# Kernel optimization log

Measured on AMD Instinct MI355X. Metric: run time of the kernel, lower is better.

The kernel has to match this reference:

```python
import jax, jax.numpy as jnp
import numpy as np

NU, NI, G, D, HD, OD = 8000, 10000, 4096, 64, 64, 64
ALPHA = 0.8      # self vs neighbor mixing in NodeApplyModule
EPS = 1e-8       # cosine-similarity denominator epsilon
NEG_BIG = -1e38  # replacement for all -inf rows


def setup_inputs() -> dict:
    key = jax.random.key(0)
    ks = jax.random.split(key, 24)
    def lin(k, o, i):
        return (jax.random.normal(k, (o, i), jnp.float32) * 0.02)
    def bias(k, o):
        return (jax.random.normal(k, (o,), jnp.float32) * 0.02)
    inp = {}
    inp["H"] = jax.random.randint(ks[0], (NU + NI, G), 0, 2, jnp.int32)
    inp["feats_weight"] = jax.random.normal(ks[1], (NU + NI, D), jnp.float32) * 0.1
    inp["num_groups"] = G
    # user SelfAttention params
    inp["u_Wq"] = lin(ks[2], HD, D); inp["u_bq"] = bias(ks[3], HD)
    inp["u_Wk"] = lin(ks[4], HD, D); inp["u_bk"] = bias(ks[5], HD)
    inp["u_Wv"] = lin(ks[6], HD, D); inp["u_bv"] = bias(ks[7], HD)
    inp["u_Ws"] = lin(ks[8], 1, NU); inp["u_bs"] = bias(ks[9], 1)
    # item SelfAttention params
    inp["i_Wq"] = lin(ks[10], HD, D); inp["i_bq"] = bias(ks[11], HD)
    inp["i_Wk"] = lin(ks[12], HD, D); inp["i_bk"] = bias(ks[13], HD)
    inp["i_Wv"] = lin(ks[14], HD, D); inp["i_bv"] = bias(ks[15], HD)
    inp["i_Ws"] = lin(ks[16], 1, NI); inp["i_bs"] = bias(ks[17], 1)
    # WeightedGCN NodeApplyModule linear: in_feats = 2*HD -> out_feats = OD
    inp["g_W"] = lin(ks[18], OD, 2 * HD); inp["g_b"] = bias(ks[19], OD)
    return inp


def _self_attention(x, mask, num_groups, Wq, bq, Wk, bk, Wv, bv, Ws, bs):
    # x: [N, D] ; mask: [N, G]
    q = x @ Wq.T + bq            # [N, HD]
    k = x @ Wk.T + bk            # [N, HD]
    v = x @ Wv.T + bv            # [N, HD]
    s = (q @ k.T) @ Ws.T + bs    # [N, 1]  (Linear(num_elem,1) over q@k.T)
    scores = jnp.broadcast_to(s.reshape(1, -1), (num_groups, x.shape[0]))  # [G, N]
    maskT = (mask == 0).T        # [G, N]
    scores = jnp.where(maskT, -jnp.inf, scores)
    all_inf = jnp.all(scores == -jnp.inf, axis=1, keepdims=True)
    scores = jnp.where(all_inf, jnp.float32(NEG_BIG), scores)
    w = jax.nn.softmax(scores, axis=1)   # [G, N]
    return w @ v, w                      # [G, HD], [G, N]


def reference(H, feats_weight, num_groups,
              u_Wq, u_bq, u_Wk, u_bk, u_Wv, u_bv, u_Ws, u_bs,
              i_Wq, i_bq, i_Wk, i_bk, i_Wv, i_bv, i_Ws, i_bs,
              g_W, g_b):
    users_feats = feats_weight[:NU]
    items_feats = feats_weight[NU:]
    users_mask = H[:NU]
    items_mask = H[NU:]

    gf_u, w_u = _self_attention(users_feats, users_mask, num_groups,
                                u_Wq, u_bq, u_Wk, u_bk, u_Wv, u_bv, u_Ws, u_bs)
    gf_i, w_i = _self_attention(items_feats, items_mask, num_groups,
                                i_Wq, i_bq, i_Wk, i_bk, i_Wv, i_bv, i_Ws, i_bs)
    # NaN scrubbing (faithful to torch.where(isnan, 0, .))
    gf_i = jnp.where(jnp.isnan(gf_i), 0.0, gf_i)
    w_i = jnp.where(jnp.isnan(w_i), 0.0, w_i)

    group_weights = jnp.concatenate([w_u, w_i], axis=1)   # [G, NU+NI]
    group_feats = jnp.concatenate([gf_u, gf_i], axis=1)   # [G, 2*HD]

    # similarity graph (cosine similarity of group weight rows)
    wp = group_weights @ group_weights.T                  # [G, G]
    norms = jnp.sqrt(jnp.sum(group_weights * group_weights, axis=1))
    l2 = 1.0 / (norms[:, None] * norms[None, :] + EPS)
    A = wp * l2  # edge weight src->dst at A[src, dst]; zero WP entries contribute 0

    # weighted mean aggregation (DGL msg/reduce: sum(w*h)/sum(w) over in-edges)
    msg = A.T @ group_feats                 # [G, 2*HD]: sum_src A[src,dst]*h[src]
    deg = jnp.sum(A, axis=0)[:, None]       # [G, 1]:   sum_src A[src,dst]
    h_neigh = jnp.where(deg > 0, msg / jnp.where(deg > 0, deg, 1.0), 0.0)

    agg = ALPHA * group_feats + (1.0 - ALPHA) * h_neigh
    out = jax.nn.sigmoid(agg @ g_W.T + g_b)               # [G, OD]
    return out
```

## Files before the change

### kernel.cpp

```cpp
#include <hip/hip_runtime.h>
#include <hip/hip_bf16.h>
#include <cstdint>
#include <cstddef>

#define NU   8000
#define NI   10000
#define NTOT 18000
#define G    4096
#define KP2  18176
#define NSL  284
#define NSL128 142
#define KT8  142
#define UT8  63
#define KP2B 2272
#define GB8  512

typedef __attribute__((ext_vector_type(4))) float f32x4;

__device__ __forceinline__ float bfu(unsigned short u){
  return __uint_as_float(((unsigned)u)<<16);
}
__device__ __forceinline__ unsigned short f2b(float f){
  __hip_bfloat16 h = __float2bfloat16(f);
  return __builtin_bit_cast(unsigned short, h);
}
__device__ __forceinline__ unsigned char f2f8(float v){
  int p = __builtin_amdgcn_cvt_pk_fp8_f32(v, 0.f, 0, false);
  return (unsigned char)(p & 0xff);
}
template<int SEL>
__device__ __forceinline__ float f8tof(unsigned int w){
  return __builtin_amdgcn_cvt_f32_fp8((int)w, SEL);
}
__device__ __forceinline__ void async16(void* lds, const void* g){
  __builtin_amdgcn_global_load_lds((const __attribute__((address_space(1))) unsigned int*)g,
                                   (__attribute__((address_space(3))) unsigned int*)lds, 16, 0, 0);
}
__device__ __forceinline__ int slot2n(int s){
  return (s < 8064) ? (s < 8000 ? s : -1) : (s-64 < NTOT ? s-64 : -1);
}
__device__ __forceinline__ unsigned int mask4(unsigned int n){
  return ((n*0x00204081u)&0x01010101u)*0xFFu;
}

__global__ __launch_bounds__(256) void k_proj(
    const float* __restrict__ feats,
    const float* uWq, const float* ubq, const float* uWk, const float* ubk,
    const float* uWv, const float* ubv, const float* uWs,
    const float* iWq, const float* ibq, const float* iWk, const float* ibk,
    const float* iWv, const float* ibv, const float* iWs,
    float* __restrict__ q, unsigned short* __restrict__ vrow, float* __restrict__ wsk)
{
  __shared__ unsigned short Wt[6*4096];
  __shared__ float bl[6*64];
  __shared__ float wacc[128];
  const float* mats[6]  = {uWq,uWk,uWv,iWq,iWk,iWv};
  const float* bias6[6] = {ubq,ubk,ubv,ibq,ibk,ibv};
  int t = threadIdx.x;
  for (int m=0;m<6;m++)
    for (int e=t; e<4096; e+=256){
      int dd = e>>6, jj = e&63;
      Wt[m*4096 + jj*64 + dd] = f2b(mats[m][e]);
    }
  for (int e=t; e<384; e+=256) bl[e] = bias6[e>>6][e&63];
  if (t<128) wacc[t]=0.f;
  __syncthreads();
  int wave=t>>6, lane=t&63;
  int gw = blockIdx.x*4+wave, nw = gridDim.x*4;
  float accU=0.f, accI=0.f;
  for (int n=gw; n<NTOT; n+=nw){
    int br = (n>=NU);
    const unsigned short* W = Wt + br*3*4096;
    const float* bb = bl + br*192;
    float x = feats[(size_t)n*64+lane];
    float qd=bb[lane], kd=bb[64+lane], vd=bb[128+lane];
    #pragma unroll 16
    for (int j=0;j<64;j++){
      float xj = __shfl(x, j, 64);
      qd += xj * bfu(W[       j*64+lane]);
      kd += xj * bfu(W[4096 + j*64+lane]);
      vd += xj * bfu(W[8192 + j*64+lane]);
    }
    q[(size_t)n*64+lane] = qd;
    vrow[(size_t)n*64+lane] = f2b(vd);
    float wsn = br ? iWs[n-NU] : uWs[n];
    if (br) accI += wsn*kd; else accU += wsn*kd;
  }
  atomicAdd(&wacc[lane], accU);
  atomicAdd(&wacc[64+lane], accI);
  __syncthreads();
  if (t<128) atomicAdd(&wsk[t], wacc[t]);
}

__global__ __launch_bounds__(256) void k_score(const float* __restrict__ q, const float* __restrict__ wsk,
    const float* ubs, const float* ibs, float* __restrict__ rfs, unsigned char* __restrict__ rbs)
{
  __shared__ float wl[128];
  __shared__ float bs2[2];
  int t=threadIdx.x;
  if (t<128) wl[t]=wsk[t];
  if (t==128) bs2[0]=ubs[0];
  if (t==129) bs2[1]=ibs[0];
  __syncthreads();
  int wave=t>>6, lane=t&63;
  #pragma unroll 4
  for (int i=0;i<32;i++){
    int slot = blockIdx.x*128 + i*4 + wave;
    int n = slot2n(slot);
    int br = (slot>=8064);
    float v = 0.f;
    if (n>=0) v = q[(size_t)n*64+lane] * wl[br*64+lane];
    #pragma unroll
    for (int m=32;m>=1;m>>=1) v += __shfl_xor(v, m, 64);
    if (lane==0){
      if (n>=0){
        unsigned char b = f2f8(expf(v + bs2[br]));
        rbs[slot]=b; rfs[slot]=f8tof<0>((unsigned int)b);
      } else {
        rbs[slot]=0; rfs[slot]=0.f;
      }
    }
  }
}

__global__ __launch_bounds__(256) void k_buildB(
    const int* __restrict__ H, const float* __restrict__ rfs,
    unsigned char* __restrict__ Wb, unsigned char* __restrict__ Wbt,
    float* __restrict__ Zu, float* __restrict__ Zi,
    float* __restrict__ S2u, float* __restrict__ S2i)
{
  __shared__ __align__(16) unsigned char Bt[128][16];
  __shared__ float rl[128];
  __shared__ float zp[16][128];
  __shared__ float sp[16][128];
  int t = threadIdx.x;
  int s0 = blockIdx.x*128, g0 = blockIdx.y*128;
  int isItem = (s0 >= 8064);
  if (t<128){ int n = slot2n(s0+t); rl[t] = (n>=0)? rfs[s0+t] : 0.f; }
  __syncthreads();
  int gb = t&15, rbase = t>>4;
  float za[8]={0.f,0.f,0.f,0.f,0.f,0.f,0.f,0.f};
  float sa[8]={0.f,0.f,0.f,0.f,0.f,0.f,0.f,0.f};
  #pragma unroll
  for (int i=0;i<8;i++){
    int row = rbase + i*16;
    int n = slot2n(s0+row);
    unsigned int b8 = 0;
    if (n>=0){
      const int* hp = H + (size_t)n*G + g0 + gb*8;
      int4 h0 = *(const int4*)hp;
      int4 h1 = *(const int4*)(hp+4);
      float rq = rl[row], rq2 = rq*rq;
      if (h0.x){ b8|=1u;    za[0]+=rq; sa[0]+=rq2; }
      if (h0.y){ b8|=2u;    za[1]+=rq; sa[1]+=rq2; }
      if (h0.z){ b8|=4u;    za[2]+=rq; sa[2]+=rq2; }
      if (h0.w){ b8|=8u;    za[3]+=rq; sa[3]+=rq2; }
      if (h1.x){ b8|=16u;   za[4]+=rq; sa[4]+=rq2; }
      if (h1.y){ b8|=32u;   za[5]+=rq; sa[5]+=rq2; }
      if (h1.z){ b8|=64u;   za[6]+=rq; sa[6]+=rq2; }
      if (h1.w){ b8|=128u;  za[7]+=rq; sa[7]+=rq2; }
    }
    Bt[row][gb] = (unsigned char)b8;
  }
  #pragma unroll
  for (int j=0;j<8;j++){ zp[rbase][gb*8+j]=za[j]; sp[rbase][gb*8+j]=sa[j]; }
  __syncthreads();
  {
    int row = t>>1, half = t&1;
    *(unsigned long long*)(Wbt + (size_t)(s0+row)*GB8 + (g0>>3) + half*8) =
        *(const unsigned long long*)(&Bt[row][half*8]);
  }
  {
    int g = t>>1, sh = t&1;
    int gB = g>>3, gs = g&7;
    unsigned long long ob = 0;
    #pragma unroll
    for (int sb=0; sb<8; sb++){
      int base = (sh*8+sb)*8;
      unsigned int x = 0;
      #pragma unroll
      for (int j=0;j<8;j++) x |= (((unsigned int)(Bt[base+j][gB]) >> gs)&1u) << j;
      ob |= (unsigned long long)x << (sb*8);
    }
    *(unsigned long long*)(Wb + (size_t)(g0+g)*KP2B + (s0>>3) + sh*8) = ob;
  }
  if (t<128){
    float z=0.f, s2=0.f;
    #pragma unroll
    for (int j=0;j<16;j++){ z += zp[j][t]; s2 += sp[j][t]; }
    if (isItem){ atomicAdd(&Zi[g0+t], z); atomicAdd(&S2i[g0+t], s2); }
    else       { atomicAdd(&Zu[g0+t], z); atomicAdd(&S2u[g0+t], s2); }
  }
}

__global__ __launch_bounds__(256) void k_mid(
    const float* __restrict__ Zu, const float* __restrict__ Zi,
    const float* __restrict__ S2u, const float* __restrict__ S2i,
    float* __restrict__ Cu, float* __restrict__ Ci,
    float* __restrict__ cnu, float* __restrict__ cni, float* __restrict__ ninv,
    unsigned char* __restrict__ cn8u, unsigned char* __restrict__ cn8i,
    unsigned char* __restrict__ Wb, unsigned char* __restrict__ Wbt,
    const unsigned short* __restrict__ vrow, unsigned char* __restrict__ vt8)
{
  __shared__ unsigned short tile[64][65];
  int b = blockIdx.x;
  int t = threadIdx.x;
  if (b == 0){
    for (int g=t; g<G; g+=256){
      float zu=Zu[g], zi=Zi[g];
      int fu = !(zu>0.f), fi = !(zi>0.f);
      float cu = fu ? (1.f/(float)NU) : 1.f/zu;
      float ci = fi ? (1.f/(float)NI) : 1.f/zi;
      float nu  = fu ? (1.f/(float)NU) : S2u[g]*cu*cu;
      float ni_ = fi ? (1.f/(float)NI) : S2i[g]*ci*ci;
      float nv = rsqrtf(nu+ni_);
      Cu[g]=cu; Ci[g]=ci; ninv[g]=nv; cnu[g]=cu*nv; cni[g]=ci*nv;
      cn8u[g] = f2f8(cu*nv*64.f);
      cn8i[g] = f2f8(ci*nv*64.f);
      if (fu){
        for (int k=0;k<1000;k++) Wb[(size_t)g*KP2B+k]=0xFF;
        for (int k=0;k<NU;k++)
          atomicOr((unsigned*)Wbt + (((size_t)k*GB8 + (g>>3))>>2), 1u<<((g&7) + 8*((g>>3)&3)));
      }
      if (fi){
        for (int k=1008;k<2258;k++) Wb[(size_t)g*KP2B+k]=0xFF;
        for (int k=8064;k<18064;k++)
          atomicOr((unsigned*)Wbt + (((size_t)k*GB8 + (g>>3))>>2), 1u<<((g&7) + 8*((g>>3)&3)));
      }
    }
    return;
  }
  int s0 = (b-1)*64;
  int tc = t&63, tr = t>>6;
  #pragma unroll
  for (int i=0;i<16;i++){
    int row = tr+i*4;
    int n = slot2n(s0+row);
    tile[row][tc] = (n>=0) ? vrow[(size_t)n*64+tc] : (unsigned short)0;
  }
  __syncthreads();
  int dOff = (s0 >= 8064) ? 64 : 0;
  #pragma unroll
  for (int i=0;i<16;i++){
    int dd = tr+i*4;
    float v = bfu(tile[tc][dd]) * 16.f;
    vt8[(size_t)(dOff+dd)*KP2 + s0+tc] = f2f8(v);
  }
}

template<int MODE>
__global__ __launch_bounds__(256) void k_gemm(
    const unsigned char* __restrict__ A, const unsigned char* __restrict__ B,
    float* __restrict__ Cs, float* __restrict__ degsl,
    const unsigned char* __restrict__ u8,
    const unsigned char* __restrict__ cn8u, const unsigned char* __restrict__ cn8i,
    float* __restrict__ uslice, const unsigned char* __restrict__ rbsg,
    long ldF, long ldc)
{
  __shared__ __align__(16) unsigned char BufF[2][16384];
  __shared__ __align__(16) unsigned char BufB[2][2048];
  __shared__ __align__(16) unsigned char AuxR[2][1024];
  __shared__ unsigned int RowDw[128];
  int t=threadIdx.x, wave=t>>6, lane=t&63;
  int I=blockIdx.x, J=blockIdx.y, z=blockIdx.z;
  int kt0=0, ktn=0;
  if (MODE==0){ kt0 = z*9; ktn = min(9, KT8-kt0); }
  else if (MODE==1){ kt0 = z*8; ktn = 8; }
  else {
    if (z<8){ kt0 = z*8;             ktn = min(8, UT8-kt0); }
    else    { kt0 = UT8 + (z-8)*10;  ktn = min(10, KT8-kt0); }
  }
  f32x4 acc[4][4];
  #pragma unroll
  for (int mi=0;mi<4;mi++)
    #pragma unroll
    for (int ni=0;ni<4;ni++){
      acc[mi][ni][0]=0.f; acc[mi][ni][1]=0.f; acc[mi][ni][2]=0.f; acc[mi][ni][3]=0.f;
    }
  f32x4 accd[4];
  if (MODE==2){
    #pragma unroll
    for (int mi=0;mi<4;mi++){ accd[mi][0]=0.f; accd[mi][1]=0.f; accd[mi][2]=0.f; accd[mi][3]=0.f; }
  }
  f32x4 accu[4];
  if (MODE==1){
    #pragma unroll
    for (int ni=0;ni<4;ni++){ accu[ni][0]=0.f; accu[ni][1]=0.f; accu[ni][2]=0.f; accu[ni][3]=0.f; }
  }
  int l7 = lane&7, q4 = lane>>4, cl15 = lane&15;
  int rowOff = wave*8 + (lane>>3);
  int cchunk = (lane&7) ^ ((lane>>3)&7);
  long aRow0 = (MODE==1) ? ((J>=UT8)?128:0) : 0;
  const unsigned char* Fbase;
  const unsigned char* Bitbase;
  if (MODE==1){ Fbase = A + aRow0*ldF + (long)cchunk*16; Bitbase = B + (long)J*128*GB8; }
  else        { Fbase = B + (long)cchunk*16;             Bitbase = A + (long)I*128*KP2B; }
  const unsigned char* cnrow = (MODE==1) ? ((J>=UT8) ? cn8i : cn8u) : nullptr;
  int mrow0 = (wave&1)*64, nrow0 = (wave>>1)*64;

  if (MODE==1 && t<128) RowDw[t] = 0x01010101u * (unsigned int)rbsg[(size_t)J*128 + t];

  auto STAGE = [&](int buf, int kt){
    long k0 = (long)kt*128;
    #pragma unroll
    for (int rr=0; rr<4; rr++)
      async16(BufF[buf] + wave*1024 + rr*4096, Fbase + (long)(rr*32 + rowOff)*ldF + k0);
    if (wave<2)
      async16(BufB[buf] + wave*1024, Bitbase + (long)(wave*64+lane)*(MODE==1?GB8:KP2B) + (long)kt*16);
    if (MODE!=1 && wave==2)
      async16(AuxR[buf], rbsg + (long)kt*128 + (long)(lane&7)*16);
  };

  STAGE(0, kt0);
  __syncthreads();

  for (int kt=kt0; kt<kt0+ktn; ++kt){
    int cur = (kt - kt0) & 1;
    if (kt+1 < kt0+ktn) STAGE(cur^1, kt+1);
    const unsigned char* Fb = BufF[cur];
    const unsigned char* Bb = BufB[cur];
    #pragma unroll
    for (int kk=0; kk<4; kk++){
      int xoff = (((kk*2 + (q4>>1)) ^ l7) << 4) + ((q4&1)<<3);
      int kb = kk*4 + q4;
      long af[4], bf[4];
      if (MODE==1){
        #pragma unroll
        for (int mi=0;mi<4;mi++)
          af[mi] = *(const long*)(Fb + (mrow0 + mi*16 + cl15)*128 + xoff);
        #pragma unroll
        for (int ni=0;ni<4;ni++){
          int row = nrow0 + ni*16 + cl15;
          unsigned int bb = Bb[row*16 + kb];
          unsigned int sp = RowDw[row];
          unsigned int lo = mask4(bb&15u)&sp, hi = mask4(bb>>4)&sp;
          bf[ni] = (long)(((unsigned long long)hi<<32)|(unsigned long long)lo);
        }
      } else {
        unsigned long long rdw = *(const unsigned long long*)(AuxR[cur] + kb*8);
        unsigned int rlo = (unsigned int)rdw, rhi = (unsigned int)(rdw>>32);
        #pragma unroll
        for (int mi=0;mi<4;mi++){
          unsigned int bb = Bb[(mrow0 + mi*16 + cl15)*16 + kb];
          unsigned int lo = mask4(bb&15u)&rlo, hi = mask4(bb>>4)&rhi;
          af[mi] = (long)(((unsigned long long)hi<<32)|(unsigned long long)lo);
        }
        #pragma unroll
        for (int ni=0;ni<4;ni++)
          bf[ni] = *(const long*)(Fb + (nrow0 + ni*16 + cl15)*128 + xoff);
      }
      #pragma unroll
      for (int mi=0;mi<4;mi++)
        #pragma unroll
        for (int ni=0;ni<4;ni++)
          acc[mi][ni] = __builtin_amdgcn_mfma_f32_16x16x32_fp8_fp8(af[mi], bf[ni], acc[mi][ni], 0,0,0);
      if (MODE==2){
        long bu = 0;
        if (cl15==0) bu = *(const long*)(u8 + (size_t)kt*128 + kk*32 + q4*8);
        #pragma unroll
        for (int mi=0;mi<4;mi++)
          accd[mi] = __builtin_amdgcn_mfma_f32_16x16x32_fp8_fp8(af[mi], bu, accd[mi], 0,0,0);
      }
      if (MODE==1){
        long au = 0;
        if (cl15==0) au = *(const long*)(cnrow + (size_t)kt*128 + kk*32 + q4*8);
        #pragma unroll
        for (int ni=0;ni<4;ni++)
          accu[ni] = __builtin_amdgcn_mfma_f32_16x16x32_fp8_fp8(au, bf[ni], accu[ni], 0,0,0);
      }
    }
    __syncthreads();
  }
  int cq = lane>>4, cl = lane&15;
  float* slice = (MODE==1) ? (Cs + (size_t)z*128*KP2) : (Cs + (size_t)z*G*128);
  #pragma unroll
  for (int mi=0;mi<4;mi++)
    #pragma unroll
    for (int ni=0;ni<4;ni++)
      #pragma unroll
      for (int rg=0;rg<4;rg++){
        int gi = (MODE==1 ? 0 : I*128) + mrow0 + mi*16 + cq*4 + rg;
        int hi = J*128 + nrow0 + ni*16 + cl;
        slice[(size_t)gi*ldc + hi] = acc[mi][ni][rg];
      }
  if (MODE==2 && (wave>>1)==0 && cl15==0){
    #pragma unroll
    for (int mi=0;mi<4;mi++)
      #pragma unroll
      for (int rg=0;rg<4;rg++){
        int gi = I*128 + mrow0 + mi*16 + cq*4 + rg;
        degsl[(size_t)z*G + gi] = accd[mi][rg];
      }
  }
  if (MODE==1 && (wave&1)==0 && q4==0){
    #pragma unroll
    for (int ni=0;ni<4;ni++){
      int si = J*128 + nrow0 + ni*16 + cl15;
      uslice[(size_t)z*KP2 + si] = accu[ni][0];
    }
  }
}

__global__ __launch_bounds__(256) void k_gfpost(const float* __restrict__ gfsl,
    const float* __restrict__ Cu, const float* __restrict__ Ci, const float* __restrict__ ninv,
    float* __restrict__ gf, unsigned char* __restrict__ gfsT2_8)
{
  __shared__ float tile[64][65];
  int g0 = blockIdx.x*64, d0 = blockIdx.y*64;
  int tc=threadIdx.x&63, tr=threadIdx.x>>6;
  const float* Cd = blockIdx.y ? Ci : Cu;
  #pragma unroll
  for (int i=0;i<16;i++){
    int rr=tr+i*4;
    size_t off = (size_t)(g0+rr)*128 + d0+tc;
    float s = 0.f;
    #pragma unroll
    for (int zz=0;zz<16;zz++) s += gfsl[(size_t)zz*G*128 + off];
    float gfv = s * Cd[g0+rr] * 0.0625f;
    gf[off] = gfv;
    tile[rr][tc] = gfv * ninv[g0+rr];
  }
  __syncthreads();
  #pragma unroll
  for (int i=0;i<16;i++){
    int dd=tr+i*4;
    float v = tile[tc][dd] * 64.f;
    int g = g0+tc;
    gfsT2_8[(size_t)(d0+dd)*G + g]     = f2f8(v*Cu[g]);
    gfsT2_8[(size_t)(128+d0+dd)*G + g] = f2f8(v*Ci[g]);
  }
}

__global__ __launch_bounds__(256) void k_red1(const float* __restrict__ tmpsl,
    unsigned char* __restrict__ tmpT8, const float* __restrict__ uslice, unsigned char* __restrict__ u8){
  int b = blockIdx.x, t = threadIdx.x;
  if (b >= 2272){
    int idx2 = (b-2272)*256 + t;
    if (idx2 < KP2/4){
      size_t off = (size_t)idx2*4;
      f32x4 s = *(const f32x4*)(uslice + off);
      #pragma unroll
      for (int z=1;z<4;z++){
        f32x4 v = *(const f32x4*)(uslice + (size_t)z*KP2 + off);
        s[0]+=v[0]; s[1]+=v[1]; s[2]+=v[2]; s[3]+=v[3];
      }
      uchar4 pk;
      pk.x = f2f8(s[0]*0.015625f);
      pk.y = f2f8(s[1]*0.015625f);
      pk.z = f2f8(s[2]*0.015625f);
      pk.w = f2f8(s[3]*0.015625f);
      *(uchar4*)(u8 + off) = pk;
    }
    return;
  }
  int idx = b*256 + t;
  int d = idx / 4544;
  int n = (idx - d*4544)*4;
  size_t off = (size_t)d*KP2 + n;
  f32x4 s = *(const f32x4*)(tmpsl + off);
  #pragma unroll
  for (int z=1;z<4;z++){
    f32x4 v = *(const f32x4*)(tmpsl + (size_t)z*128*KP2 + off);
    s[0]+=v[0]; s[1]+=v[1]; s[2]+=v[2]; s[3]+=v[3];
  }
  uchar4 pk;
  pk.x = f2f8(s[0]); pk.y = f2f8(s[1]); pk.z = f2f8(s[2]); pk.w = f2f8(s[3]);
  *(uchar4*)(tmpT8 + off) = pk;
}

__global__ __launch_bounds__(256) void k_final(const float* __restrict__ gf, const float* __restrict__ msgsl,
    const float* __restrict__ degsl, const float* __restrict__ cnu, const float* __restrict__ cni,
    const float* __restrict__ gW, const float* __restrict__ gb, float* __restrict__ out)
{
  __shared__ float Wl[64*129];
  __shared__ float aggL[4][128];
  __shared__ float gbL[64];
  __shared__ float degL[4];
  int t=threadIdx.x;
  for (int e=t; e<8192; e+=256){ int o=e>>7, dd=e&127; Wl[o*129+dd] = gW[e]; }
  if (t<64) gbL[t] = gb[t];
  int g0 = blockIdx.x*4;
  if (t<4){
    int g = g0+t;
    float su=0.f, si=0.f;
    #pragma unroll
    for (int z=0;z<8;z++) su += degsl[(size_t)z*G + g];
    #pragma unroll
    for (int z=8;z<16;z++) si += degsl[(size_t)z*G + g];
    degL[t] = cnu[g]*su + cni[g]*si;
  }
  __syncthreads();
  for (int e=t; e<512; e+=256){
    int gl=e>>7, dd=e&127; int g=g0+gl;
    size_t off = (size_t)g*128 + dd;
    float su=0.f, si=0.f;
    #pragma unroll
    for (int z=0;z<8;z++)  su += msgsl[(size_t)z*G*128 + off];
    #pragma unroll
    for (int z=8;z<16;z++) si += msgsl[(size_t)z*G*128 + off];
    float mv = (cnu[g]*su + cni[g]*si)*0.015625f;
    float dv = degL[gl];
    float hn = dv>0.f ? mv/dv : 0.f;
    aggL[gl][dd] = 0.8f*gf[off] + 0.2f*hn;
  }
  __syncthreads();
  int gl = t>>6, o = t&63;
  float s = gbL[o];
  #pragma unroll
  for (int dd=0; dd<128; dd++) s += aggL[gl][dd]*Wl[o*129+dd];
  out[(size_t)(g0+gl)*64 + o] = 1.f/(1.f+expf(-s));
}

extern "C" void kernel_launch(void* const* d_in, const int* in_sizes, int n_in,
                              void* d_out, int out_size, void* d_ws, size_t ws_size,
                              hipStream_t stream)
{
  (void)in_sizes; (void)n_in; (void)out_size; (void)ws_size;
  const int* H = (const int*)d_in[0];
  const float* feats = (const float*)d_in[1];
  const float* uWq=(const float*)d_in[3];
  const float* ubq=(const float*)d_in[4];
  const float* uWk=(const float*)d_in[5];
  const float* ubk=(const float*)d_in[6];
  const float* uWv=(const float*)d_in[7];
  const float* ubv=(const float*)d_in[8];
  const float* uWs=(const float*)d_in[9];
  const float* ubs=(const float*)d_in[10];
  const float* iWq=(const float*)d_in[11];
  const float* ibq=(const float*)d_in[12];
  const float* iWk=(const float*)d_in[13];
  const float* ibk=(const float*)d_in[14];
  const float* iWv=(const float*)d_in[15];
  const float* ibv=(const float*)d_in[16];
  const float* iWs=(const float*)d_in[17];
  const float* ibs=(const float*)d_in[18];
  const float* gW =(const float*)d_in[19];
  const float* gb =(const float*)d_in[20];
  float* out = (float*)d_out;

  char* p = (char*)d_ws;
  auto alloc=[&](size_t b)->void*{ void* r=(void*)p; p += (b+255)&~(size_t)255; return r; };
  char* zbase = p;
  float* wsk  = (float*)alloc(128*4);
  float* Zu   = (float*)alloc(G*4);
  float* Zi   = (float*)alloc(G*4);
  float* S2u  = (float*)alloc(G*4);
  float* S2i  = (float*)alloc(G*4);
  unsigned char* vt8 = (unsigned char*)alloc((size_t)128*KP2);
  size_t zlen = (size_t)(p - zbase);
  unsigned char* Wb    = (unsigned char*)alloc((size_t)G*KP2B);
  unsigned char* Wbt   = (unsigned char*)alloc((size_t)KP2*GB8);
  unsigned char* tmpT8 = (unsigned char*)alloc((size_t)128*KP2);
  unsigned char* gfsT2_8=(unsigned char*)alloc((size_t)256*G);
  float* slb  = (float*)alloc((size_t)4*128*KP2*4);
  float* uslice=(float*)alloc((size_t)4*KP2*4);
  float* degsl= (float*)alloc((size_t)16*G*4);
  float* gf   = (float*)alloc((size_t)G*128*4);
  float* q    = (float*)alloc((size_t)NTOT*64*4);
  unsigned short* vrow=(unsigned short*)alloc((size_t)NTOT*64*2);
  float* rfs  = (float*)alloc((size_t)KP2*4);
  unsigned char* rbs = (unsigned char*)alloc((size_t)KP2);
  float* Cu   = (float*)alloc(G*4);
  float* Ci   = (float*)alloc(G*4);
  float* cnu  = (float*)alloc(G*4);
  float* cni  = (float*)alloc(G*4);
  float* ninv = (float*)alloc(G*4);
  unsigned char* cn8u = (unsigned char*)alloc(G);
  unsigned char* cn8i = (unsigned char*)alloc(G);
  unsigned char* u8 = (unsigned char*)alloc((size_t)KP2);

  (void)hipMemsetAsync(zbase, 0, zlen, stream);

  k_proj<<<256,256,0,stream>>>(feats, uWq,ubq,uWk,ubk,uWv,ubv,uWs,
                               iWq,ibq,iWk,ibk,iWv,ibv,iWs, q, vrow, wsk);
  k_score<<<KP2/128,256,0,stream>>>(q, wsk, ubs, ibs, rfs, rbs);
  k_buildB<<<dim3(NSL128,32),256,0,stream>>>(H, rfs, Wb, Wbt, Zu, Zi, S2u, S2i);
  k_mid<<<NSL+1,256,0,stream>>>(Zu,Zi,S2u,S2i,Cu,Ci,cnu,cni,ninv,cn8u,cn8i,Wb,Wbt,vrow,vt8);
  k_gemm<0><<<dim3(32,1,16),256,0,stream>>>(Wb, vt8, slb, nullptr, nullptr, nullptr, nullptr, nullptr,
                                            rbs, (long)KP2, 128);
  k_gfpost<<<dim3(64,2),256,0,stream>>>(slb, Cu, Ci, ninv, gf, gfsT2_8);
  k_gemm<1><<<dim3(1,KT8,4),256,0,stream>>>(gfsT2_8, Wbt, slb, nullptr, nullptr, cn8u, cn8i, uslice,
                                            rbs, (long)G, (long)KP2);
  k_red1<<<2272+18,256,0,stream>>>(slb, tmpT8, uslice, u8);
  k_gemm<2><<<dim3(32,1,16),256,0,stream>>>(Wb, tmpT8, slb, degsl, u8, nullptr, nullptr, nullptr,
                                            rbs, (long)KP2, 128);
  k_final<<<G/4,256,0,stream>>>(gf, slb, degsl, cnu, cni, gW, gb, out);
}
```

Before: 682.7 us.

## Fold Q/K projection algebraically and fuse reduction kernels via last-block counters

The score s = (q·k^T)·Ws collapses to a linear function of x, so k_proj now computes only V plus the sums Σws·x and Σws, and k_score derives a combined 64-vector from Wk and Wq to score each row directly from feats. This drops the q buffer and the Q/K matmuls. The separate k_mid, k_gfpost and k_red1 launches are folded into the tails of k_buildB, k_score and the k_gemm modes, using atomic arrival counters so the last block performs each reduction. This cuts launches and intermediate traffic, but serializes the tail work onto one block per group and relies on threadfence/counter correctness.

```diff
diff --git a/kernel.cpp b/kernel.cpp
--- a/kernel.cpp
+++ b/kernel.cpp
@@ -8,7 +8,6 @@
 #define NTOT 18000
 #define G    4096
 #define KP2  18176
-#define NSL  284
 #define NSL128 142
 #define KT8  142
 #define UT8  63
@@ -45,80 +44,121 @@
 
 __global__ __launch_bounds__(256) void k_proj(
     const float* __restrict__ feats,
-    const float* uWq, const float* ubq, const float* uWk, const float* ubk,
     const float* uWv, const float* ubv, const float* uWs,
-    const float* iWq, const float* ibq, const float* iWk, const float* ibk,
     const float* iWv, const float* ibv, const float* iWs,
-    float* __restrict__ q, unsigned short* __restrict__ vrow, float* __restrict__ wsk)
+    unsigned short* __restrict__ vrow, float* __restrict__ suG)
 {
-  __shared__ unsigned short Wt[6*4096];
-  __shared__ float bl[6*64];
-  __shared__ float wacc[128];
-  const float* mats[6]  = {uWq,uWk,uWv,iWq,iWk,iWv};
-  const float* bias6[6] = {ubq,ubk,ubv,ibq,ibk,ibv};
+  __shared__ unsigned short Wt[2*4096];
+  __shared__ float bl[2*64];
+  __shared__ float sacc[130];
+  const float* mats[2]  = {uWv,iWv};
+  const float* bias2[2] = {ubv,ibv};
   int t = threadIdx.x;
-  for (int m=0;m<6;m++)
+  for (int m=0;m<2;m++)
     for (int e=t; e<4096; e+=256){
       int dd = e>>6, jj = e&63;
       Wt[m*4096 + jj*64 + dd] = f2b(mats[m][e]);
     }
-  for (int e=t; e<384; e+=256) bl[e] = bias6[e>>6][e&63];
-  if (t<128) wacc[t]=0.f;
+  for (int e=t; e<128; e+=256) bl[e] = bias2[e>>6][e&63];
+  if (t<130) sacc[t]=0.f;
   __syncthreads();
   int wave=t>>6, lane=t&63;
   int gw = blockIdx.x*4+wave, nw = gridDim.x*4;
-  float accU=0.f, accI=0.f;
+  float accU=0.f, accI=0.f, swsU=0.f, swsI=0.f;
   for (int n=gw; n<NTOT; n+=nw){
     int br = (n>=NU);
-    const unsigned short* W = Wt + br*3*4096;
-    const float* bb = bl + br*192;
+    const unsigned short* W = Wt + br*4096;
     float x = feats[(size_t)n*64+lane];
-    float qd=bb[lane], kd=bb[64+lane], vd=bb[128+lane];
+    float vd = bl[br*64+lane];
     #pragma unroll 16
     for (int j=0;j<64;j++){
       float xj = __shfl(x, j, 64);
-      qd += xj * bfu(W[       j*64+lane]);
-      kd += xj * bfu(W[4096 + j*64+lane]);
-      vd += xj * bfu(W[8192 + j*64+lane]);
-    }
-    q[(size_t)n*64+lane] = qd;
+      vd += xj * bfu(W[j*64+lane]);
+    }
     vrow[(size_t)n*64+lane] = f2b(vd);
     float wsn = br ? iWs[n-NU] : uWs[n];
-    if (br) accI += wsn*kd; else accU += wsn*kd;
-  }
-  atomicAdd(&wacc[lane], accU);
-  atomicAdd(&wacc[64+lane], accI);
-  __syncthreads();
-  if (t<128) atomicAdd(&wsk[t], wacc[t]);
-}
-
-__global__ __launch_bounds__(256) void k_score(const float* __restrict__ q, const float* __restrict__ wsk,
-    const float* ubs, const float* ibs, float* __restrict__ rfs, unsigned char* __restrict__ rbs)
+    if (br){ accI += wsn*x; swsI += wsn; } else { accU += wsn*x; swsU += wsn; }
+  }
+  atomicAdd(&sacc[lane], accU);
+  atomicAdd(&sacc[64+lane], accI);
+  if (lane==0){ atomicAdd(&sacc[128], swsU); atomicAdd(&sacc[129], swsI); }
+  __syncthreads();
+  if (t<130) atomicAdd(&suG[t], sacc[t]);
+}
+
+__global__ __launch_bounds__(256) void k_score(
+    const float* __restrict__ feats, const float* __restrict__ suG,
+    const float* uWq, const float* ubq, const float* uWk, const float* ubk, const float* ubs,
+    const float* iWq, const float* ibq, const float* iWk, const float* ibk, const float* ibs,
+    const unsigned short* __restrict__ vrow,
+    float* __restrict__ rfs, unsigned char* __restrict__ rbs, unsigned char* __restrict__ vt8)
 {
-  __shared__ float wl[128];
-  __shared__ float bs2[2];
-  int t=threadIdx.x;
-  if (t<128) wl[t]=wsk[t];
-  if (t==128) bs2[0]=ubs[0];
-  if (t==129) bs2[1]=ibs[0];
-  __syncthreads();
-  int wave=t>>6, lane=t&63;
+  __shared__ float suL[130];
+  __shared__ float wskL[128];
+  __shared__ float w2L[128];
+  __shared__ float cL[2];
+  __shared__ unsigned short tile[64][65];
+  int t=threadIdx.x, wave=t>>6, lane=t&63;
+  if (t<130) suL[t]=suG[t];
+  __syncthreads();
+  if (wave<2){
+    const float* Wk = wave? iWk : uWk;
+    const float* bk = wave? ibk : ubk;
+    const float* su = suL + wave*64;
+    float a = suL[128+wave]*bk[lane];
+    #pragma unroll 8
+    for (int j=0;j<64;j++) a += su[j]*Wk[lane*64+j];
+    wskL[wave*64+lane] = a;
+  }
+  __syncthreads();
+  if (wave<2){
+    const float* Wq = wave? iWq : uWq;
+    const float* bq = wave? ibq : ubq;
+    const float* wk = wskL + wave*64;
+    float a = 0.f;
+    #pragma unroll 8
+    for (int d=0; d<64; d++) a += wk[d]*Wq[(size_t)d*64+lane];
+    w2L[wave*64+lane] = a;
+    float cp = wk[lane]*bq[lane];
+    #pragma unroll
+    for (int m=32;m>=1;m>>=1) cp += __shfl_xor(cp, m, 64);
+    if (lane==0) cL[wave] = cp + (wave? ibs[0] : ubs[0]);
+  }
+  __syncthreads();
+  int s0 = blockIdx.x*128;
+  int br = (s0>=8064);
   #pragma unroll 4
   for (int i=0;i<32;i++){
-    int slot = blockIdx.x*128 + i*4 + wave;
+    int slot = s0 + i*4 + wave;
     int n = slot2n(slot);
-    int br = (slot>=8064);
     float v = 0.f;
-    if (n>=0) v = q[(size_t)n*64+lane] * wl[br*64+lane];
+    if (n>=0) v = feats[(size_t)n*64+lane] * w2L[br*64+lane];
     #pragma unroll
     for (int m=32;m>=1;m>>=1) v += __shfl_xor(v, m, 64);
     if (lane==0){
       if (n>=0){
-        unsigned char b = f2f8(expf(v + bs2[br]));
+        unsigned char b = f2f8(expf(v + cL[br]));
         rbs[slot]=b; rfs[slot]=f8tof<0>((unsigned int)b);
-      } else {
-        rbs[slot]=0; rfs[slot]=0.f;
-      }
+      } else { rbs[slot]=0; rfs[slot]=0.f; }
+    }
+  }
+  int dOff = br ? 64 : 0;
+  int tc = t&63, tr = t>>6;
+  for (int h=0; h<2; h++){
+    int sb = s0 + h*64;
+    __syncthreads();
+    #pragma unroll
+    for (int i=0;i<16;i++){
+      int row = tr+i*4;
+      int n = slot2n(sb+row);
+      tile[row][tc] = (n>=0) ? vrow[(size_t)n*64+tc] : (unsigned short)0;
+    }
+    __syncthreads();
+    #pragma unroll
+    for (int i=0;i<16;i++){
+      int dd = tr+i*4;
+      float v = bfu(tile[tc][dd]) * 16.f;
+      vt8[(size_t)(dOff+dd)*KP2 + sb+tc] = f2f8(v);
     }
   }
 }
@@ -127,12 +167,17 @@
     const int* __restrict__ H, const float* __restrict__ rfs,
     unsigned char* __restrict__ Wb, unsigned char* __restrict__ Wbt,
     float* __restrict__ Zu, float* __restrict__ Zi,
-    float* __restrict__ S2u, float* __restrict__ S2i)
+    float* __restrict__ S2u, float* __restrict__ S2i,
+    unsigned int* __restrict__ cntB,
+    float* __restrict__ Cu, float* __restrict__ Ci,
+    float* __restrict__ cnu, float* __restrict__ cni, float* __restrict__ ninv,
+    unsigned char* __restrict__ cn8u, unsigned char* __restrict__ cn8i)
 {
   __shared__ __align__(16) unsigned char Bt[128][16];
   __shared__ float rl[128];
   __shared__ float zp[16][128];
   __shared__ float sp[16][128];
+  __shared__ unsigned lf;
   int t = threadIdx.x;
   int s0 = blockIdx.x*128, g0 = blockIdx.y*128;
   int isItem = (s0 >= 8064);
@@ -191,60 +236,32 @@
     if (isItem){ atomicAdd(&Zi[g0+t], z); atomicAdd(&S2i[g0+t], s2); }
     else       { atomicAdd(&Zu[g0+t], z); atomicAdd(&S2u[g0+t], s2); }
   }
-}
-
-__global__ __launch_bounds__(256) void k_mid(
-    const float* __restrict__ Zu, const float* __restrict__ Zi,
-    const float* __restrict__ S2u, const float* __restrict__ S2i,
-    float* __restrict__ Cu, float* __restrict__ Ci,
-    float* __restrict__ cnu, float* __restrict__ cni, float* __restrict__ ninv,
-    unsigned char* __restrict__ cn8u, unsigned char* __restrict__ cn8i,
-    unsigned char* __restrict__ Wb, unsigned char* __restrict__ Wbt,
-    const unsigned short* __restrict__ vrow, unsigned char* __restrict__ vt8)
-{
-  __shared__ unsigned short tile[64][65];
-  int b = blockIdx.x;
-  int t = threadIdx.x;
-  if (b == 0){
-    for (int g=t; g<G; g+=256){
-      float zu=Zu[g], zi=Zi[g];
-      int fu = !(zu>0.f), fi = !(zi>0.f);
-      float cu = fu ? (1.f/(float)NU) : 1.f/zu;
-      float ci = fi ? (1.f/(float)NI) : 1.f/zi;
-      float nu  = fu ? (1.f/(float)NU) : S2u[g]*cu*cu;
-      float ni_ = fi ? (1.f/(float)NI) : S2i[g]*ci*ci;
-      float nv = rsqrtf(nu+ni_);
-      Cu[g]=cu; Ci[g]=ci; ninv[g]=nv; cnu[g]=cu*nv; cni[g]=ci*nv;
-      cn8u[g] = f2f8(cu*nv*64.f);
-      cn8i[g] = f2f8(ci*nv*64.f);
-      if (fu){
-        for (int k=0;k<1000;k++) Wb[(size_t)g*KP2B+k]=0xFF;
-        for (int k=0;k<NU;k++)
-          atomicOr((unsigned*)Wbt + (((size_t)k*GB8 + (g>>3))>>2), 1u<<((g&7) + 8*((g>>3)&3)));
-      }
-      if (fi){
-        for (int k=1008;k<2258;k++) Wb[(size_t)g*KP2B+k]=0xFF;
-        for (int k=8064;k<18064;k++)
-          atomicOr((unsigned*)Wbt + (((size_t)k*GB8 + (g>>3))>>2), 1u<<((g&7) + 8*((g>>3)&3)));
-      }
-    }
-    return;
-  }
-  int s0 = (b-1)*64;
-  int tc = t&63, tr = t>>6;
-  #pragma unroll
-  for (int i=0;i<16;i++){
-    int row = tr+i*4;
-    int n = slot2n(s0+row);
-    tile[row][tc] = (n>=0) ? vrow[(size_t)n*64+tc] : (unsigned short)0;
-  }
-  __syncthreads();
-  int dOff = (s0 >= 8064) ? 64 : 0;
-  #pragma unroll
-  for (int i=0;i<16;i++){
-    int dd = tr+i*4;
-    float v = bfu(tile[tc][dd]) * 16.f;
-    vt8[(size_t)(dOff+dd)*KP2 + s0+tc] = f2f8(v);
+  __threadfence();
+  if (t==0) lf = atomicAdd(cntB, 1u);
+  __syncthreads();
+  if (lf != (unsigned)(NSL128*32-1)) return;
+  __threadfence();
+  for (int g=t; g<G; g+=256){
+    float zu=Zu[g], zi=Zi[g];
+    int fu = !(zu>0.f), fi = !(zi>0.f);
+    float cu = fu ? (1.f/(float)NU) : 1.f/zu;
+    float ci = fi ? (1.f/(float)NI) : 1.f/zi;
+    float nu  = fu ? (1.f/(float)NU) : S2u[g]*cu*cu;
+    float ni_ = fi ? (1.f/(float)NI) : S2i[g]*ci*ci;
+    float nv = rsqrtf(nu+ni_);
+    Cu[g]=cu; Ci[g]=ci; ninv[g]=nv; cnu[g]=cu*nv; cni[g]=ci*nv;
+    cn8u[g] = f2f8(cu*nv*64.f);
+    cn8i[g] = f2f8(ci*nv*64.f);
+    if (fu){
+      for (int k=0;k<1000;k++) Wb[(size_t)g*KP2B+k]=0xFF;
+      for (int k=0;k<NU;k++)
+        atomicOr((unsigned*)Wbt + (((size_t)k*GB8 + (g>>3))>>2), 1u<<((g&7) + 8*((g>>3)&3)));
+    }
+    if (fi){
+      for (int k=1008;k<2258;k++) Wb[(size_t)g*KP2B+k]=0xFF;
+      for (int k=8064;k<18064;k++)
+        atomicOr((unsigned*)Wbt + (((size_t)k*GB8 + (g>>3))>>2), 1u<<((g&7) + 8*((g>>3)&3)));
+    }
   }
 }
 
@@ -255,12 +272,17 @@
     const unsigned char* __restrict__ u8,
     const unsigned char* __restrict__ cn8u, const unsigned char* __restrict__ cn8i,
     float* __restrict__ uslice, const unsigned char* __restrict__ rbsg,
+    unsigned int* __restrict__ cnt,
+    const float* __restrict__ Cu, const float* __restrict__ Ci, const float* __restrict__ ninv,
+    float* __restrict__ gf, unsigned char* __restrict__ gfsT2_8,
+    unsigned char* __restrict__ tmpT8o, unsigned char* __restrict__ u8o,
     long ldF, long ldc)
 {
   __shared__ __align__(16) unsigned char BufF[2][16384];
   __shared__ __align__(16) unsigned char BufB[2][2048];
   __shared__ __align__(16) unsigned char AuxR[2][1024];
   __shared__ unsigned int RowDw[128];
+  __shared__ unsigned lfs;
   int t=threadIdx.x, wave=t>>6, lane=t&63;
   int I=blockIdx.x, J=blockIdx.y, z=blockIdx.z;
   int kt0=0, ktn=0;
@@ -399,73 +421,74 @@
       uslice[(size_t)z*KP2 + si] = accu[ni][0];
     }
   }
-}
-
-__global__ __launch_bounds__(256) void k_gfpost(const float* __restrict__ gfsl,
-    const float* __restrict__ Cu, const float* __restrict__ Ci, const float* __restrict__ ninv,
-    float* __restrict__ gf, unsigned char* __restrict__ gfsT2_8)
-{
-  __shared__ float tile[64][65];
-  int g0 = blockIdx.x*64, d0 = blockIdx.y*64;
-  int tc=threadIdx.x&63, tr=threadIdx.x>>6;
-  const float* Cd = blockIdx.y ? Ci : Cu;
-  #pragma unroll
-  for (int i=0;i<16;i++){
-    int rr=tr+i*4;
-    size_t off = (size_t)(g0+rr)*128 + d0+tc;
-    float s = 0.f;
-    #pragma unroll
-    for (int zz=0;zz<16;zz++) s += gfsl[(size_t)zz*G*128 + off];
-    float gfv = s * Cd[g0+rr] * 0.0625f;
-    gf[off] = gfv;
-    tile[rr][tc] = gfv * ninv[g0+rr];
-  }
-  __syncthreads();
-  #pragma unroll
-  for (int i=0;i<16;i++){
-    int dd=tr+i*4;
-    float v = tile[tc][dd] * 64.f;
-    int g = g0+tc;
-    gfsT2_8[(size_t)(d0+dd)*G + g]     = f2f8(v*Cu[g]);
-    gfsT2_8[(size_t)(128+d0+dd)*G + g] = f2f8(v*Ci[g]);
-  }
-}
-
-__global__ __launch_bounds__(256) void k_red1(const float* __restrict__ tmpsl,
-    unsigned char* __restrict__ tmpT8, const float* __restrict__ uslice, unsigned char* __restrict__ u8){
-  int b = blockIdx.x, t = threadIdx.x;
-  if (b >= 2272){
-    int idx2 = (b-2272)*256 + t;
-    if (idx2 < KP2/4){
-      size_t off = (size_t)idx2*4;
-      f32x4 s = *(const f32x4*)(uslice + off);
+
+  if (MODE==0){
+    __threadfence();
+    if (t==0) lfs = atomicAdd(cnt+I, 1u);
+    __syncthreads();
+    if (lfs != 15u) return;
+    __threadfence();
+    float (*ftile)[65] = (float(*)[65])(&BufF[0][0]);
+    int tc=t&63, tr=t>>6;
+    for (int gh=0; gh<2; gh++){
+      int g0 = I*128 + gh*64;
+      for (int dh=0; dh<2; dh++){
+        int d0 = dh*64;
+        const float* Cd = dh ? Ci : Cu;
+        __syncthreads();
+        #pragma unroll
+        for (int i=0;i<16;i++){
+          int rr=tr+i*4;
+          size_t off = (size_t)(g0+rr)*128 + d0+tc;
+          float s = 0.f;
+          #pragma unroll
+          for (int zz=0; zz<16; zz++) s += Cs[(size_t)zz*G*128 + off];
+          float gfv = s * Cd[g0+rr] * 0.0625f;
+          gf[off] = gfv;
+          ftile[rr][tc] = gfv * ninv[g0+rr];
+        }
+        __syncthreads();
+        #pragma unroll
+        for (int i=0;i<16;i++){
+          int dd=tr+i*4;
+          float v = ftile[tc][dd] * 64.f;
+          int g = g0+tc;
+          gfsT2_8[(size_t)(d0+dd)*G + g]     = f2f8(v*Cu[g]);
+          gfsT2_8[(size_t)(128+d0+dd)*G + g] = f2f8(v*Ci[g]);
+        }
+      }
+    }
+  }
+  if (MODE==1){
+    __threadfence();
+    if (t==0) lfs = atomicAdd(cnt+J, 1u);
+    __syncthreads();
+    if (lfs != 3u) return;
+    __threadfence();
+    #pragma unroll
+    for (int i=0;i<16;i++){
+      int idx = i*256 + t;
+      int d = idx>>5;
+      int cq2 = (idx&31)*4;
+      size_t off = (size_t)d*KP2 + J*128 + cq2;
+      f32x4 s = *(const f32x4*)(Cs + off);
       #pragma unroll
-      for (int z=1;z<4;z++){
-        f32x4 v = *(const f32x4*)(uslice + (size_t)z*KP2 + off);
+      for (int zz=1; zz<4; zz++){
+        f32x4 v = *(const f32x4*)(Cs + (size_t)zz*128*KP2 + off);
         s[0]+=v[0]; s[1]+=v[1]; s[2]+=v[2]; s[3]+=v[3];
       }
       uchar4 pk;
-      pk.x = f2f8(s[0]*0.015625f);
-      pk.y = f2f8(s[1]*0.015625f);
-      pk.z = f2f8(s[2]*0.015625f);
-      pk.w = f2f8(s[3]*0.015625f);
-      *(uchar4*)(u8 + off) = pk;
-    }
-    return;
-  }
-  int idx = b*256 + t;
-  int d = idx / 4544;
-  int n = (idx - d*4544)*4;
-  size_t off = (size_t)d*KP2 + n;
-  f32x4 s = *(const f32x4*)(tmpsl + off);
-  #pragma unroll
-  for (int z=1;z<4;z++){
-    f32x4 v = *(const f32x4*)(tmpsl + (size_t)z*128*KP2 + off);
-    s[0]+=v[0]; s[1]+=v[1]; s[2]+=v[2]; s[3]+=v[3];
-  }
-  uchar4 pk;
-  pk.x = f2f8(s[0]); pk.y = f2f8(s[1]); pk.z = f2f8(s[2]); pk.w = f2f8(s[3]);
-  *(uchar4*)(tmpT8 + off) = pk;
+      pk.x=f2f8(s[0]); pk.y=f2f8(s[1]); pk.z=f2f8(s[2]); pk.w=f2f8(s[3]);
+      *(uchar4*)(tmpT8o + off) = pk;
+    }
+    if (t<128){
+      int si = J*128 + t;
+      float s = 0.f;
+      #pragma unroll
+      for (int zz=0; zz<4; zz++) s += uslice[(size_t)zz*KP2 + si];
+      u8o[si] = f2f8(s*0.015625f);
+    }
+  }
 }
 
 __global__ __launch_bounds__(256) void k_final(const float* __restrict__ gf, const float* __restrict__ msgsl,
@@ -541,11 +564,14 @@
   char* p = (char*)d_ws;
   auto alloc=[&](size_t b)->void*{ void* r=(void*)p; p += (b+255)&~(size_t)255; return r; };
   char* zbase = p;
-  float* wsk  = (float*)alloc(128*4);
+  float* suG  = (float*)alloc(130*4);
   float* Zu   = (float*)alloc(G*4);
   float* Zi   = (float*)alloc(G*4);
   float* S2u  = (float*)alloc(G*4);
   float* S2i  = (float*)alloc(G*4);
+  unsigned int* cnt0 = (unsigned int*)alloc(32*4);
+  unsigned int* cnt1 = (unsigned int*)alloc(142*4);
+  unsigned int* cntB = (unsigned int*)alloc(4);
   unsigned char* vt8 = (unsigned char*)alloc((size_t)128*KP2);
   size_t zlen = (size_t)(p - zbase);
   unsigned char* Wb    = (unsigned char*)alloc((size_t)G*KP2B);
@@ -556,7 +582,6 @@
   float* uslice=(float*)alloc((size_t)4*KP2*4);
   float* degsl= (float*)alloc((size_t)16*G*4);
   float* gf   = (float*)alloc((size_t)G*128*4);
-  float* q    = (float*)alloc((size_t)NTOT*64*4);
   unsigned short* vrow=(unsigned short*)alloc((size_t)NTOT*64*2);
   float* rfs  = (float*)alloc((size_t)KP2*4);
   unsigned char* rbs = (unsigned char*)alloc((size_t)KP2);
@@ -571,18 +596,19 @@
 
   (void)hipMemsetAsync(zbase, 0, zlen, stream);
 
-  k_proj<<<256,256,0,stream>>>(feats, uWq,ubq,uWk,ubk,uWv,ubv,uWs,
-                               iWq,ibq,iWk,ibk,iWv,ibv,iWs, q, vrow, wsk);
-  k_score<<<KP2/128,256,0,stream>>>(q, wsk, ubs, ibs, rfs, rbs);
-  k_buildB<<<dim3(NSL128,32),256,0,stream>>>(H, rfs, Wb, Wbt, Zu, Zi, S2u, S2i);
-  k_mid<<<NSL+1,256,0,stream>>>(Zu,Zi,S2u,S2i,Cu,Ci,cnu,cni,ninv,cn8u,cn8i,Wb,Wbt,vrow,vt8);
+  k_proj<<<256,256,0,stream>>>(feats, uWv,ubv,uWs, iWv,ibv,iWs, vrow, suG);
+  k_score<<<KP2/128,256,0,stream>>>(feats, suG, uWq,ubq,uWk,ubk,ubs,
+                                    iWq,ibq,iWk,ibk,ibs, vrow, rfs, rbs, vt8);
+  k_buildB<<<dim3(NSL128,32),256,0,stream>>>(H, rfs, Wb, Wbt, Zu, Zi, S2u, S2i,
+                                             cntB, Cu, Ci, cnu, cni, ninv, cn8u, cn8i);
   k_gemm<0><<<dim3(32,1,16),256,0,stream>>>(Wb, vt8, slb, nullptr, nullptr, nullptr, nullptr, nullptr,
-                                            rbs, (long)KP2, 128);
-  k_gfpost<<<dim3(64,2),256,0,stream>>>(slb, Cu, Ci, ninv, gf, gfsT2_8);
+                                            rbs, cnt0, Cu, Ci, ninv, gf, gfsT2_8, nullptr, nullptr,
+                                            (long)KP2, 128);
   k_gemm<1><<<dim3(1,KT8,4),256,0,stream>>>(gfsT2_8, Wbt, slb, nullptr, nullptr, cn8u, cn8i, uslice,
-                                            rbs, (long)G, (long)KP2);
-  k_red1<<<2272+18,256,0,stream>>>(slb, tmpT8, uslice, u8);
+                                            rbs, cnt1, nullptr, nullptr, nullptr, nullptr, nullptr,
+                                            tmpT8, u8, (long)G, (long)KP2);
   k_gemm<2><<<dim3(32,1,16),256,0,stream>>>(Wb, tmpT8, slb, degsl, u8, nullptr, nullptr, nullptr,
-                                            rbs, (long)KP2, 128);
+                                            rbs, nullptr, nullptr, nullptr, nullptr, nullptr, nullptr,
+                                            nullptr, nullptr, (long)KP2, 128);
   k_final<<<G/4,256,0,stream>>>(gf, slb, degsl, cnu, cni, gW, gb, out);
 }
```

After: 1.818 ms. 166% more time.
